# Kernel tuning notes

Measured on AMD Instinct MI355X. Metric: run time of the kernel, lower is better.

The kernel has to match this reference:

```python
import jax, jax.numpy as jnp
import numpy as np
from jax import lax

B, CIN, COUT, H, W, K = 8, 64, 64, 96, 96, 3
PAD = K // 2
EPS = 1e-5


def _conv(x, w, pad):
    return lax.conv_general_dilated(x, w, window_strides=(1, 1),
                                    padding=[(pad, pad), (pad, pad)],
                                    dimension_numbers=('NCHW', 'OIHW', 'NCHW'))


def setup_inputs() -> dict:
    key = jax.random.key(0)
    ks = jax.random.split(key, 7)
    x = jax.random.normal(ks[0], (B, CIN, H, W), dtype=jnp.float32)
    # offset conv (zero-init in the original; use small random weights so offsets are nontrivial)
    w_off = jax.random.normal(ks[1], (2 * K * K, CIN, K, K), dtype=jnp.float32) * 0.01
    b_off = jax.random.normal(ks[2], (2 * K * K,), dtype=jnp.float32) * 0.01
    w_def = jax.random.normal(ks[3], (COUT, CIN, K, K), dtype=jnp.float32) * (1.0 / np.sqrt(CIN * K * K))
    b_def = jax.random.normal(ks[4], (COUT,), dtype=jnp.float32) * 0.01
    gamma = jax.random.normal(ks[5], (COUT,), dtype=jnp.float32) * 0.1 + 1.0
    beta = jax.random.normal(ks[6], (COUT,), dtype=jnp.float32) * 0.1
    return {"x": x, "w_off": w_off, "b_off": b_off, "w_def": w_def,
            "b_def": b_def, "gamma": gamma, "beta": beta}


def _deform_block(x, w_off, b_off, w_def, b_def, gamma, beta):
    # 1) predict offsets: [B, 2*K*K, H, W]; channel 2k = dy, 2k+1 = dx for tap k=ky*K+kx
    offset = _conv(x, w_off, PAD) + b_off[None, :, None, None]
    dy = offset[:, 0::2]  # [B, K*K, H, W]
    dx = offset[:, 1::2]

    # 2) sampling positions p = p0 + p_k + dp (stride 1, zero-padding semantics)
    yy = jnp.arange(H, dtype=jnp.float32)[:, None]          # [H,1]
    xx = jnp.arange(W, dtype=jnp.float32)[None, :]          # [1,W]
    kk = jnp.arange(K * K)
    ky = (kk // K - PAD).astype(jnp.float32)[None, :, None, None]
    kx = (kk % K - PAD).astype(jnp.float32)[None, :, None, None]
    py = yy[None, None] + ky + dy                            # [B, K*K, H, W]
    px = xx[None, None] + kx + dx

    # 3) bilinear gather with zero outside-boundary
    y0 = jnp.floor(py); x0 = jnp.floor(px)
    ly = py - y0; lx = px - x0
    x_flat = x.reshape(B, CIN, H * W)
    sampled = jnp.zeros((B, CIN, K * K, H, W), dtype=x.dtype)
    for iy, wy in ((y0, 1.0 - ly), (y0 + 1.0, ly)):
        for ix, wx in ((x0, 1.0 - lx), (x0 + 1.0, lx)):
            valid = (iy >= 0) & (iy < H) & (ix >= 0) & (ix < W)
            yi = jnp.clip(iy, 0, H - 1).astype(jnp.int32)
            xi = jnp.clip(ix, 0, W - 1).astype(jnp.int32)
            idx = (yi * W + xi).reshape(B, -1)               # [B, K*K*H*W]
            vals = jnp.take_along_axis(x_flat, idx[:, None, :], axis=2)
            vals = vals.reshape(B, CIN, K * K, H, W)
            wgt = (wy * wx * valid.astype(x.dtype))[:, None]  # [B,1,K*K,H,W]
            sampled = sampled + vals * wgt

    # 4) deformable conv = contraction of sampled taps with kernel weights
    out = jnp.einsum('bckhw,ock->bohw', sampled, w_def.reshape(COUT, CIN, K * K))
    out = out + b_def[None, :, None, None]

    # 5) BatchNorm (training-mode batch statistics) + ReLU
    mean = jnp.mean(out, axis=(0, 2, 3))
    var = jnp.var(out, axis=(0, 2, 3))
    out = (out - mean[None, :, None, None]) * lax.rsqrt(var + EPS)[None, :, None, None]
    out = out * gamma[None, :, None, None] + beta[None, :, None, None]
    return jax.nn.relu(out)


def reference(x, w_off, b_off, w_def, b_def, gamma, beta):
    return _deform_block(x, w_off, b_off, w_def, b_def, gamma, beta)
```

## Files before the change

### kernel.cpp

```cpp
#include <hip/hip_runtime.h>

#define Hh 96
#define Ww 96
#define CIN 64
#define COUT 64
#define BATCH 8
#define HW 9216
#define NOFF 18

#define XS_ROW   13824
#define XS_SIZE  124416
#define WS_BASE  124416
#define OF_BASE  147744
#define SM_TOTAL 159264

typedef __attribute__((ext_vector_type(8))) short bf16x8;
typedef __attribute__((ext_vector_type(4))) float f32x4;

__device__ inline ushort f2bf(float f) {
  union { float f; uint u; } v; v.f = f;
  uint u = v.u;
  u += 0x7FFF + ((u >> 16) & 1);
  return (ushort)(u >> 16);
}
__device__ inline float bf2f(ushort s) {
  union { uint u; float f; } v; v.u = ((uint)s) << 16; return v.f;
}
__device__ inline float bflo(uint u) {
  union { uint u; float f; } v; v.u = u << 16; return v.f;
}
__device__ inline float bfhi(uint u) {
  union { uint u; float f; } v; v.u = u & 0xFFFF0000u; return v.f;
}
__device__ inline uint cvtpk(float lo, float hi) {
  uint r;
  asm("v_cvt_pk_bf16_f32 %0, %1, %2" : "=v"(r) : "v"(lo), "v"(hi));
  return r;
}
__device__ inline uint interp_pack(uint p00, uint p01, uint p10, uint p11,
                                   float w00, float w01, float w10, float w11) {
  float vlo = fmaf(w11, bflo(p11), fmaf(w10, bflo(p10),
              fmaf(w01, bflo(p01), w00 * bflo(p00))));
  float vhi = fmaf(w11, bfhi(p11), fmaf(w10, bfhi(p10),
              fmaf(w01, bfhi(p01), w00 * bfhi(p00))));
  return cvtpk(vlo, vhi);
}

__global__ __launch_bounds__(256) void k_xt(
    const float* __restrict__ x, const float* __restrict__ w_def,
    const float* __restrict__ w_off, ushort* __restrict__ xt,
    ushort* __restrict__ wtb, ushort* __restrict__ wob)
{
  __shared__ float tile[64][65];
  int tid = threadIdx.x;
  int blk = blockIdx.x;

  if (blk < 9) {
    for (int i = tid; i < 4096; i += 256) {
      int o = i >> 6, c = i & 63;
      wtb[blk * 4096 + i] = f2bf(w_def[(o * 64 + c) * 9 + blk]);
    }
  } else if (blk < 25 && blk >= 16) {
    int k = blk - 16;
    for (int i = tid; i < 2048; i += 256) {
      int n = i >> 6, c = i & 63;
      wob[k * 2048 + i] = (n < NOFF) ? f2bf(w_off[(n * 64 + c) * 9 + k]) : (ushort)0;
    }
  }

  int b = blk / 144;
  int pbase = (blk - b * 144) * 64;
  int wave = tid >> 6, lane = tid & 63;
  const float* xp = x + (size_t)b * CIN * HW + pbase;
  #pragma unroll
  for (int i = 0; i < 16; ++i) {
    int c = wave * 16 + i;
    tile[lane][c] = xp[(size_t)c * HW + lane];
  }
  __syncthreads();
  ushort* xo = xt + ((size_t)b * HW + pbase) * 64;
  #pragma unroll
  for (int i = 0; i < 16; ++i) {
    int p = wave * 16 + i;
    xo[(size_t)p * 64 + lane] = f2bf(tile[p][lane]);
  }
}

__global__ __launch_bounds__(768, 3) void k_main(
    const ushort* __restrict__ xt, const ushort* __restrict__ wtb,
    const ushort* __restrict__ wob, const float* __restrict__ b_off,
    const float* __restrict__ b_def, float* __restrict__ out,
    float* __restrict__ parts)
{
  extern __shared__ char sm[];
  int tid = threadIdx.x;
  int bid = blockIdx.x;
  int b = bid & 7;
  int rt = bid >> 3;
  int r0 = rt * 3;

  {
    const ushort* xsrc = xt + (size_t)b * HW * 64;
    for (int q = tid; q < 6912; q += 768) {
      int s = q / 768;
      int rem = q - s * 768;
      int cxp = rem >> 3, c16 = rem & 7;
      int srow = min(max(r0 - 3 + s, 0), 95);
      uint4 v = *(const uint4*)(xsrc + (size_t)(srow * 96 + cxp) * 64 + c16 * 8);
      *(uint4*)(sm + s * XS_ROW + cxp * 144 + c16 * 16) = v;
    }
  }
  for (int q = tid; q < 1296; q += 768) {
    int k = q / 144;
    int rem = q - k * 144;
    int n = rem >> 3, c16 = rem & 7;
    uint4 v = *(const uint4*)(wob + k * 2048 + n * 64 + c16 * 8);
    *(uint4*)(sm + WS_BASE + k * 2592 + n * 144 + c16 * 16) = v;
  }
  __syncthreads();

  int wave = tid >> 6, lane = tid & 63;
  int m = lane & 15, hi = lane >> 4;
  int kh = wave & 1;
  int gb = wave >> 1;
  int khB = kh * 64, hiB = hi * 16;

  int hA[3], wAc[3], pPix[3], gV[3];
  #pragma unroll
  for (int ti = 0; ti < 3; ++ti) {
    int g = gb + ti * 6;
    gV[ti] = g;
    int gr = g / 6, gc = g - gr * 6;
    hA[ti] = r0 + gr;
    wAc[ti] = gc * 16 + m;
    pPix[ti] = g * 16 + m;
  }

  f32x4 oacc[3][2];
  #pragma unroll
  for (int ti = 0; ti < 3; ++ti) {
    oacc[ti][0] = (f32x4){0.f, 0.f, 0.f, 0.f};
    oacc[ti][1] = (f32x4){0.f, 0.f, 0.f, 0.f};
  }
  for (int k = 0; k < 9; ++k) {
    int ky = k / 3 - 1, kx = (k - (k / 3) * 3) - 1;
    const char* wkb = sm + WS_BASE + k * 2592;
    bf16x8 wb0 = *(const bf16x8*)(wkb + m * 144 + hiB + khB);
    int r1 = min(16 + m, 17);
    bf16x8 wb1 = *(const bf16x8*)(wkb + r1 * 144 + hiB + khB);
    #pragma unroll
    for (int ti = 0; ti < 3; ++ti) {
      int yy = hA[ti] + ky, xx = wAc[ti] + kx;
      bool valid = (yy >= 0 && yy < Hh && xx >= 0 && xx < Ww);
      int cy = min(max(yy, 0), 95), cx = min(max(xx, 0), 95);
      int sy = cy - r0 + 3;
      bf16x8 a = *(const bf16x8*)(sm + sy * XS_ROW + cx * 144 + hiB + khB);
      if (!valid) a = (bf16x8)0;
      oacc[ti][0] = __builtin_amdgcn_mfma_f32_16x16x32_bf16(a, wb0, oacc[ti][0], 0, 0, 0);
      oacc[ti][1] = __builtin_amdgcn_mfma_f32_16x16x32_bf16(a, wb1, oacc[ti][1], 0, 0, 0);
    }
  }

  int j0 = m, j1 = 16 + m;
  if (kh == 1) {
    #pragma unroll
    for (int ti = 0; ti < 3; ++ti) {
      #pragma unroll
      for (int r = 0; r < 4; ++r) {
        int p = gV[ti] * 16 + hi * 4 + r;
        *(ushort*)(sm + OF_BASE + p * 40 + j0 * 2) = f2bf(oacc[ti][0][r]);
        if (m < 2)
          *(ushort*)(sm + OF_BASE + p * 40 + j1 * 2) = f2bf(oacc[ti][1][r]);
      }
    }
  }
  __syncthreads();
  if (kh == 0) {
    float bo0 = b_off[j0];
    float bo1 = (m < 2) ? b_off[j1] : 0.f;
    #pragma unroll
    for (int ti = 0; ti < 3; ++ti) {
      #pragma unroll
      for (int r = 0; r < 4; ++r) {
        int p = gV[ti] * 16 + hi * 4 + r;
        ushort* a0p = (ushort*)(sm + OF_BASE + p * 40 + j0 * 2);
        *a0p = f2bf(oacc[ti][0][r] + bf2f(*a0p) + bo0);
        if (m < 2) {
          ushort* a1p = (ushort*)(sm + OF_BASE + p * 40 + j1 * 2);
          *a1p = f2bf(oacc[ti][1][r] + bf2f(*a1p) + bo1);
        }
      }
    }
  }
  if (tid < 512) {
    int o = tid >> 3, c16 = tid & 7;
    uint4 v = *(const uint4*)(wtb + o * 64 + c16 * 8);
    *(uint4*)(sm + WS_BASE + o * 144 + c16 * 16) = v;
  }
  __syncthreads();

  f32x4 acc[3][4];
  #pragma unroll
  for (int ti = 0; ti < 3; ++ti)
    #pragma unroll
    for (int nt = 0; nt < 4; ++nt) acc[ti][nt] = (f32x4){0.f, 0.f, 0.f, 0.f};

  for (int k = 0; k < 9; ++k) {
    if (k < 8 && tid < 512) {
      int o = tid >> 3, c16 = tid & 7;
      uint4 v = *(const uint4*)(wtb + (k + 1) * 4096 + o * 64 + c16 * 8);
      *(uint4*)(sm + WS_BASE + ((k + 1) & 1) * 9216 + o * 144 + c16 * 16) = v;
    }
    int ky = k / 3 - 1, kx = (k - (k / 3) * 3) - 1;
    const char* wkb = sm + WS_BASE + (k & 1) * 9216;
    bf16x8 bf0 = *(const bf16x8*)(wkb + m * 144 + hiB + khB);
    bf16x8 bf1 = *(const bf16x8*)(wkb + (16 + m) * 144 + hiB + khB);
    bf16x8 bf2 = *(const bf16x8*)(wkb + (32 + m) * 144 + hiB + khB);
    bf16x8 bf3 = *(const bf16x8*)(wkb + (48 + m) * 144 + hiB + khB);

    #pragma unroll
    for (int ti = 0; ti < 3; ++ti) {
      uint dd = *(const uint*)(sm + OF_BASE + pPix[ti] * 40 + k * 4);
      float dy = bflo(dd), dx = bfhi(dd);
      float py = (float)(hA[ti] + ky) + dy;
      float px = (float)(wAc[ti] + kx) + dx;
      float y0f = floorf(py), x0f = floorf(px);
      float ly = py - y0f, lx = px - x0f;
      int y0 = (int)y0f, x0 = (int)x0f;
      int y1 = y0 + 1, x1 = x0 + 1;
      float fy0 = (y0 >= 0 && y0 < Hh) ? 1.f : 0.f;
      float fy1 = (y1 >= 0 && y1 < Hh) ? 1.f : 0.f;
      float fx0 = (x0 >= 0 && x0 < Ww) ? 1.f : 0.f;
      float fx1 = (x1 >= 0 && x1 < Ww) ? 1.f : 0.f;
      int cy0 = min(max(y0, 0), 95), cy1 = min(max(y1, 0), 95);
      int cx0 = min(max(x0, 0), 95), cx1 = min(max(x1, 0), 95);
      int sy0 = min(max(cy0 - r0 + 3, 0), 8);
      int sy1 = min(max(cy1 - r0 + 3, 0), 8);
      const char* row0 = sm + sy0 * XS_ROW;
      const char* row1 = sm + sy1 * XS_ROW;
      uint4 c00 = *(const uint4*)(row0 + cx0 * 144 + hiB + khB);
      uint4 c01 = *(const uint4*)(row0 + cx1 * 144 + hiB + khB);
      uint4 c10 = *(const uint4*)(row1 + cx0 * 144 + hiB + khB);
      uint4 c11 = *(const uint4*)(row1 + cx1 * 144 + hiB + khB);
      float w00 = (1.f - ly) * (1.f - lx) * (fy0 * fx0);
      float w01 = (1.f - ly) * lx * (fy0 * fx1);
      float w10 = ly * (1.f - lx) * (fy1 * fx0);
      float w11 = ly * lx * (fy1 * fx1);
      uint ua[4];
      ua[0] = interp_pack(c00.x, c01.x, c10.x, c11.x, w00, w01, w10, w11);
      ua[1] = interp_pack(c00.y, c01.y, c10.y, c11.y, w00, w01, w10, w11);
      ua[2] = interp_pack(c00.z, c01.z, c10.z, c11.z, w00, w01, w10, w11);
      ua[3] = interp_pack(c00.w, c01.w, c10.w, c11.w, w00, w01, w10, w11);
      bf16x8 av;
      __builtin_memcpy(&av, ua, 16);
      acc[ti][0] = __builtin_amdgcn_mfma_f32_16x16x32_bf16(av, bf0, acc[ti][0], 0, 0, 0);
      acc[ti][1] = __builtin_amdgcn_mfma_f32_16x16x32_bf16(av, bf1, acc[ti][1], 0, 0, 0);
      acc[ti][2] = __builtin_amdgcn_mfma_f32_16x16x32_bf16(av, bf2, acc[ti][2], 0, 0, 0);
      acc[ti][3] = __builtin_amdgcn_mfma_f32_16x16x32_bf16(av, bf3, acc[ti][3], 0, 0, 0);
    }
    __syncthreads();
  }

  float* T = (float*)sm;
  if (kh == 1) {
    #pragma unroll
    for (int ti = 0; ti < 3; ++ti)
      #pragma unroll
      for (int nt = 0; nt < 4; ++nt) {
        int o = nt * 16 + m;
        #pragma unroll
        for (int r = 0; r < 4; ++r) {
          int p = gV[ti] * 16 + hi * 4 + r;
          T[o * 289 + p] = acc[ti][nt][r];
        }
      }
  }
  __syncthreads();
  if (kh == 0) {
    float bd[4];
    bd[0] = b_def[m]; bd[1] = b_def[16 + m];
    bd[2] = b_def[32 + m]; bd[3] = b_def[48 + m];
    #pragma unroll
    for (int ti = 0; ti < 3; ++ti)
      #pragma unroll
      for (int nt = 0; nt < 4; ++nt) {
        int o = nt * 16 + m;
        #pragma unroll
        for (int r = 0; r < 4; ++r) {
          int p = gV[ti] * 16 + hi * 4 + r;
          T[o * 289 + p] += acc[ti][nt][r] + bd[nt];
        }
      }
  }
  __syncthreads();
  if (tid < 512) {
    int o = tid >> 3, seg = tid & 7;
    const float* Tr = T + o * 289 + seg * 36;
    float* og = out + ((size_t)(b * 64 + o)) * HW + rt * 288 + seg * 36;
    float s = 0.f, ss = 0.f;
    #pragma unroll
    for (int j4 = 0; j4 < 9; ++j4) {
      float4 v;
      v.x = Tr[j4 * 4 + 0]; v.y = Tr[j4 * 4 + 1];
      v.z = Tr[j4 * 4 + 2]; v.w = Tr[j4 * 4 + 3];
      s += v.x + v.y + v.z + v.w;
      ss += v.x * v.x + v.y * v.y + v.z * v.z + v.w * v.w;
      *(float4*)(og + j4 * 4) = v;
    }
    s += __shfl_down(s, 4); s += __shfl_down(s, 2); s += __shfl_down(s, 1);
    ss += __shfl_down(ss, 4); ss += __shfl_down(ss, 2); ss += __shfl_down(ss, 1);
    if ((tid & 7) == 0) {
      parts[o * 256 + bid] = s;
      parts[16384 + o * 256 + bid] = ss;
    }
  }
}

__global__ __launch_bounds__(256) void k_stats(
    const float* __restrict__ parts, const float* __restrict__ gamma,
    const float* __restrict__ beta, float* __restrict__ stats)
{
  int c = blockIdx.x;
  int tid = threadIdx.x;
  float s = 0.f, ss = 0.f;
  for (int i = tid; i < 256; i += 256) {
    s += parts[c * 256 + i];
    ss += parts[16384 + c * 256 + i];
  }
  #pragma unroll
  for (int off = 32; off >= 1; off >>= 1) {
    s += __shfl_down(s, off);
    ss += __shfl_down(ss, off);
  }
  __shared__ float rs[4], rss[4];
  int wave = tid >> 6, lane = tid & 63;
  if (lane == 0) { rs[wave] = s; rss[wave] = ss; }
  __syncthreads();
  if (tid == 0) {
    float S1 = rs[0] + rs[1] + rs[2] + rs[3];
    float S2 = rss[0] + rss[1] + rss[2] + rss[3];
    const float inv = 1.f / 73728.f;
    float mean = S1 * inv;
    float var = S2 * inv - mean * mean;
    float scale = gamma[c] * rsqrtf(var + 1e-5f);
    stats[c] = scale;
    stats[64 + c] = beta[c] - mean * scale;
  }
}

__global__ __launch_bounds__(256) void k_norm(
    float* __restrict__ out, const float* __restrict__ stats)
{
  int g = blockIdx.x * 256 + threadIdx.x;
  int o = (g / 2304) & 63;
  float sc = stats[o], sh = stats[64 + o];
  float4 v = ((const float4*)out)[g];
  v.x = fmaxf(fmaf(v.x, sc, sh), 0.f);
  v.y = fmaxf(fmaf(v.y, sc, sh), 0.f);
  v.z = fmaxf(fmaf(v.z, sc, sh), 0.f);
  v.w = fmaxf(fmaf(v.w, sc, sh), 0.f);
  ((float4*)out)[g] = v;
}

extern "C" void kernel_launch(void* const* d_in, const int* in_sizes, int n_in,
                              void* d_out, int out_size, void* d_ws, size_t ws_size,
                              hipStream_t stream) {
  const float* x     = (const float*)d_in[0];
  const float* w_off = (const float*)d_in[1];
  const float* b_off = (const float*)d_in[2];
  const float* w_def = (const float*)d_in[3];
  const float* b_def = (const float*)d_in[4];
  const float* gamma = (const float*)d_in[5];
  const float* beta  = (const float*)d_in[6];
  float* out = (float*)d_out;

  float* base  = (float*)d_ws;
  ushort* wtb  = (ushort*)base;
  ushort* wob  = (ushort*)(base + 18432);
  ushort* xt   = (ushort*)(base + 18432 + 9216);
  float* parts = base + 18432 + 9216 + 2359296;
  float* stats = parts + 32768;

  (void)hipFuncSetAttribute((const void*)k_main,
      hipFuncAttributeMaxDynamicSharedMemorySize, SM_TOTAL);

  k_xt<<<1152, 256, 0, stream>>>(x, w_def, w_off, xt, wtb, wob);
  k_main<<<256, 768, SM_TOTAL, stream>>>(xt, wtb, wob, b_off, b_def, out, parts);
  k_stats<<<64, 256, 0, stream>>>(parts, gamma, beta, stats);
  k_norm<<<4608, 256, 0, stream>>>(out, stats);
}
```

Measured before the change: 59.95 us.

## Fuse NCHW-to-bf16 transpose into main kernel and read weights from global

Drops the separate transpose kernel that wrote a channels-last bf16 copy of x. The main kernel now loads fp32 x straight from NCHW global memory, converts it to bf16 and stores it into its shared-memory tile. Weight fragments for both the offset and the deform convolutions are read directly from global memory instead of being staged through shared memory, which frees LDS and removes the per-tap barrier. The bilinear interpolation now uses packed fp32 FMA instructions. The trade-offs are strided per-channel global loads during staging and weight reads that depend on cache hits.

```diff
diff --git a/kernel.cpp b/kernel.cpp
--- a/kernel.cpp
+++ b/kernel.cpp
@@ -10,12 +10,12 @@
 
 #define XS_ROW   13824
 #define XS_SIZE  124416
-#define WS_BASE  124416
-#define OF_BASE  147744
-#define SM_TOTAL 159264
+#define OF_BASE  124416
+#define SM_TOTAL 135936
 
 typedef __attribute__((ext_vector_type(8))) short bf16x8;
 typedef __attribute__((ext_vector_type(4))) float f32x4;
+typedef __attribute__((ext_vector_type(2))) float f32x2;
 
 __device__ inline ushort f2bf(float f) {
   union { float f; uint u; } v; v.f = f;
@@ -26,68 +26,45 @@
 __device__ inline float bf2f(ushort s) {
   union { uint u; float f; } v; v.u = ((uint)s) << 16; return v.f;
 }
-__device__ inline float bflo(uint u) {
-  union { uint u; float f; } v; v.u = u << 16; return v.f;
-}
-__device__ inline float bfhi(uint u) {
-  union { uint u; float f; } v; v.u = u & 0xFFFF0000u; return v.f;
-}
 __device__ inline uint cvtpk(float lo, float hi) {
   uint r;
   asm("v_cvt_pk_bf16_f32 %0, %1, %2" : "=v"(r) : "v"(lo), "v"(hi));
   return r;
 }
-__device__ inline uint interp_pack(uint p00, uint p01, uint p10, uint p11,
-                                   float w00, float w01, float w10, float w11) {
-  float vlo = fmaf(w11, bflo(p11), fmaf(w10, bflo(p10),
-              fmaf(w01, bflo(p01), w00 * bflo(p00))));
-  float vhi = fmaf(w11, bfhi(p11), fmaf(w10, bfhi(p10),
-              fmaf(w01, bfhi(p01), w00 * bfhi(p00))));
-  return cvtpk(vlo, vhi);
-}
-
-__global__ __launch_bounds__(256) void k_xt(
-    const float* __restrict__ x, const float* __restrict__ w_def,
-    const float* __restrict__ w_off, ushort* __restrict__ xt,
+__device__ inline f32x2 unpack2(uint u) {
+  union { uint u[2]; f32x2 f; } r;
+  r.u[0] = u << 16; r.u[1] = u & 0xFFFF0000u;
+  return r.f;
+}
+__device__ inline f32x2 pkfma(f32x2 a, f32x2 b, f32x2 c) {
+  f32x2 d;
+  asm("v_pk_fma_f32 %0, %1, %2, %3" : "=v"(d) : "v"(a), "v"(b), "v"(c));
+  return d;
+}
+__device__ inline f32x2 pkmul(f32x2 a, f32x2 b) {
+  f32x2 d;
+  asm("v_pk_mul_f32 %0, %1, %2" : "=v"(d) : "v"(a), "v"(b));
+  return d;
+}
+
+__global__ __launch_bounds__(256) void k_wpack(
+    const float* __restrict__ w_def, const float* __restrict__ w_off,
     ushort* __restrict__ wtb, ushort* __restrict__ wob)
 {
-  __shared__ float tile[64][65];
-  int tid = threadIdx.x;
-  int blk = blockIdx.x;
-
-  if (blk < 9) {
-    for (int i = tid; i < 4096; i += 256) {
-      int o = i >> 6, c = i & 63;
-      wtb[blk * 4096 + i] = f2bf(w_def[(o * 64 + c) * 9 + blk]);
-    }
-  } else if (blk < 25 && blk >= 16) {
-    int k = blk - 16;
-    for (int i = tid; i < 2048; i += 256) {
-      int n = i >> 6, c = i & 63;
-      wob[k * 2048 + i] = (n < NOFF) ? f2bf(w_off[(n * 64 + c) * 9 + k]) : (ushort)0;
-    }
-  }
-
-  int b = blk / 144;
-  int pbase = (blk - b * 144) * 64;
-  int wave = tid >> 6, lane = tid & 63;
-  const float* xp = x + (size_t)b * CIN * HW + pbase;
-  #pragma unroll
-  for (int i = 0; i < 16; ++i) {
-    int c = wave * 16 + i;
-    tile[lane][c] = xp[(size_t)c * HW + lane];
-  }
-  __syncthreads();
-  ushort* xo = xt + ((size_t)b * HW + pbase) * 64;
-  #pragma unroll
-  for (int i = 0; i < 16; ++i) {
-    int p = wave * 16 + i;
-    xo[(size_t)p * 64 + lane] = f2bf(tile[p][lane]);
+  int g = blockIdx.x * 256 + threadIdx.x;
+  if (g < 36864) {
+    int k = g >> 12, o = (g >> 6) & 63, c = g & 63;
+    wtb[g] = f2bf(w_def[(o * 64 + c) * 9 + k]);
+  }
+  int g2 = g - 36864;
+  if (g2 >= 0 && g2 < 18432) {
+    int k = g2 >> 11, n = (g2 >> 6) & 31, c = g2 & 63;
+    wob[g2] = (n < NOFF) ? f2bf(w_off[(n * 64 + c) * 9 + k]) : (ushort)0;
   }
 }
 
 __global__ __launch_bounds__(768, 3) void k_main(
-    const ushort* __restrict__ xt, const ushort* __restrict__ wtb,
+    const float* __restrict__ x, const ushort* __restrict__ wtb,
     const ushort* __restrict__ wob, const float* __restrict__ b_off,
     const float* __restrict__ b_def, float* __restrict__ out,
     float* __restrict__ parts)
@@ -100,22 +77,20 @@
   int r0 = rt * 3;
 
   {
-    const ushort* xsrc = xt + (size_t)b * HW * 64;
-    for (int q = tid; q < 6912; q += 768) {
-      int s = q / 768;
-      int rem = q - s * 768;
-      int cxp = rem >> 3, c16 = rem & 7;
+    const float* xb_g = x + (size_t)b * CIN * HW;
+    int px = tid >> 3, cg = tid & 7;
+    #pragma unroll
+    for (int s = 0; s < 9; ++s) {
       int srow = min(max(r0 - 3 + s, 0), 95);
-      uint4 v = *(const uint4*)(xsrc + (size_t)(srow * 96 + cxp) * 64 + c16 * 8);
-      *(uint4*)(sm + s * XS_ROW + cxp * 144 + c16 * 16) = v;
-    }
-  }
-  for (int q = tid; q < 1296; q += 768) {
-    int k = q / 144;
-    int rem = q - k * 144;
-    int n = rem >> 3, c16 = rem & 7;
-    uint4 v = *(const uint4*)(wob + k * 2048 + n * 64 + c16 * 8);
-    *(uint4*)(sm + WS_BASE + k * 2592 + n * 144 + c16 * 16) = v;
+      const float* src = xb_g + (size_t)(cg * 8) * HW + srow * 96 + px;
+      float v[8];
+      #pragma unroll
+      for (int j = 0; j < 8; ++j) v[j] = src[(size_t)j * HW];
+      uint u[4];
+      u[0] = cvtpk(v[0], v[1]); u[1] = cvtpk(v[2], v[3]);
+      u[2] = cvtpk(v[4], v[5]); u[3] = cvtpk(v[6], v[7]);
+      *(uint4*)(sm + s * XS_ROW + px * 144 + cg * 16) = *(uint4*)u;
+    }
   }
   __syncthreads();
 
@@ -124,6 +99,7 @@
   int kh = wave & 1;
   int gb = wave >> 1;
   int khB = kh * 64, hiB = hi * 16;
+  int chE = kh * 32 + hi * 8;
 
   int hA[3], wAc[3], pPix[3], gV[3];
   #pragma unroll
@@ -144,10 +120,9 @@
   }
   for (int k = 0; k < 9; ++k) {
     int ky = k / 3 - 1, kx = (k - (k / 3) * 3) - 1;
-    const char* wkb = sm + WS_BASE + k * 2592;
-    bf16x8 wb0 = *(const bf16x8*)(wkb + m * 144 + hiB + khB);
-    int r1 = min(16 + m, 17);
-    bf16x8 wb1 = *(const bf16x8*)(wkb + r1 * 144 + hiB + khB);
+    const ushort* wk = wob + k * 2048 + chE;
+    bf16x8 wb0 = *(const bf16x8*)(wk + m * 64);
+    bf16x8 wb1 = *(const bf16x8*)(wk + (16 + m) * 64);
     #pragma unroll
     for (int ti = 0; ti < 3; ++ti) {
       int yy = hA[ti] + ky, xx = wAc[ti] + kx;
@@ -192,11 +167,6 @@
       }
     }
   }
-  if (tid < 512) {
-    int o = tid >> 3, c16 = tid & 7;
-    uint4 v = *(const uint4*)(wtb + o * 64 + c16 * 8);
-    *(uint4*)(sm + WS_BASE + o * 144 + c16 * 16) = v;
-  }
   __syncthreads();
 
   f32x4 acc[3][4];
@@ -206,24 +176,19 @@
     for (int nt = 0; nt < 4; ++nt) acc[ti][nt] = (f32x4){0.f, 0.f, 0.f, 0.f};
 
   for (int k = 0; k < 9; ++k) {
-    if (k < 8 && tid < 512) {
-      int o = tid >> 3, c16 = tid & 7;
-      uint4 v = *(const uint4*)(wtb + (k + 1) * 4096 + o * 64 + c16 * 8);
-      *(uint4*)(sm + WS_BASE + ((k + 1) & 1) * 9216 + o * 144 + c16 * 16) = v;
-    }
     int ky = k / 3 - 1, kx = (k - (k / 3) * 3) - 1;
-    const char* wkb = sm + WS_BASE + (k & 1) * 9216;
-    bf16x8 bf0 = *(const bf16x8*)(wkb + m * 144 + hiB + khB);
-    bf16x8 bf1 = *(const bf16x8*)(wkb + (16 + m) * 144 + hiB + khB);
-    bf16x8 bf2 = *(const bf16x8*)(wkb + (32 + m) * 144 + hiB + khB);
-    bf16x8 bf3 = *(const bf16x8*)(wkb + (48 + m) * 144 + hiB + khB);
+    const ushort* wk = wtb + k * 4096 + chE;
+    bf16x8 bf0 = *(const bf16x8*)(wk + m * 64);
+    bf16x8 bf1 = *(const bf16x8*)(wk + (16 + m) * 64);
+    bf16x8 bf2 = *(const bf16x8*)(wk + (32 + m) * 64);
+    bf16x8 bf3 = *(const bf16x8*)(wk + (48 + m) * 64);
 
     #pragma unroll
     for (int ti = 0; ti < 3; ++ti) {
       uint dd = *(const uint*)(sm + OF_BASE + pPix[ti] * 40 + k * 4);
-      float dy = bflo(dd), dx = bfhi(dd);
-      float py = (float)(hA[ti] + ky) + dy;
-      float px = (float)(wAc[ti] + kx) + dx;
+      f32x2 dpair = unpack2(dd);
+      float py = (float)(hA[ti] + ky) + dpair.x;
+      float px = (float)(wAc[ti] + kx) + dpair.y;
       float y0f = floorf(py), x0f = floorf(px);
       float ly = py - y0f, lx = px - x0f;
       int y0 = (int)y0f, x0 = (int)x0f;
@@ -242,15 +207,25 @@
       uint4 c01 = *(const uint4*)(row0 + cx1 * 144 + hiB + khB);
       uint4 c10 = *(const uint4*)(row1 + cx0 * 144 + hiB + khB);
       uint4 c11 = *(const uint4*)(row1 + cx1 * 144 + hiB + khB);
-      float w00 = (1.f - ly) * (1.f - lx) * (fy0 * fx0);
-      float w01 = (1.f - ly) * lx * (fy0 * fx1);
-      float w10 = ly * (1.f - lx) * (fy1 * fx0);
-      float w11 = ly * lx * (fy1 * fx1);
+      float s00 = (1.f - ly) * (1.f - lx) * (fy0 * fx0);
+      float s01 = (1.f - ly) * lx * (fy0 * fx1);
+      float s10 = ly * (1.f - lx) * (fy1 * fx0);
+      float s11 = ly * lx * (fy1 * fx1);
+      f32x2 w00 = (f32x2){s00, s00}, w01 = (f32x2){s01, s01};
+      f32x2 w10 = (f32x2){s10, s10}, w11 = (f32x2){s11, s11};
       uint ua[4];
-      ua[0] = interp_pack(c00.x, c01.x, c10.x, c11.x, w00, w01, w10, w11);
-      ua[1] = interp_pack(c00.y, c01.y, c10.y, c11.y, w00, w01, w10, w11);
-      ua[2] = interp_pack(c00.z, c01.z, c10.z, c11.z, w00, w01, w10, w11);
-      ua[3] = interp_pack(c00.w, c01.w, c10.w, c11.w, w00, w01, w10, w11);
+      {
+        const uint* p00 = (const uint*)&c00; const uint* p01 = (const uint*)&c01;
+        const uint* p10 = (const uint*)&c10; const uint* p11 = (const uint*)&c11;
+        #pragma unroll
+        for (int q = 0; q < 4; ++q) {
+          f32x2 sv = pkmul(w00, unpack2(p00[q]));
+          sv = pkfma(w01, unpack2(p01[q]), sv);
+          sv = pkfma(w10, unpack2(p10[q]), sv);
+          sv = pkfma(w11, unpack2(p11[q]), sv);
+          ua[q] = cvtpk(sv.x, sv.y);
+        }
+      }
       bf16x8 av;
       __builtin_memcpy(&av, ua, 16);
       acc[ti][0] = __builtin_amdgcn_mfma_f32_16x16x32_bf16(av, bf0, acc[ti][0], 0, 0, 0);
@@ -258,8 +233,8 @@
       acc[ti][2] = __builtin_amdgcn_mfma_f32_16x16x32_bf16(av, bf2, acc[ti][2], 0, 0, 0);
       acc[ti][3] = __builtin_amdgcn_mfma_f32_16x16x32_bf16(av, bf3, acc[ti][3], 0, 0, 0);
     }
-    __syncthreads();
-  }
+  }
+  __syncthreads();
 
   float* T = (float*)sm;
   if (kh == 1) {
@@ -323,9 +298,9 @@
   int c = blockIdx.x;
   int tid = threadIdx.x;
   float s = 0.f, ss = 0.f;
-  for (int i = tid; i < 256; i += 256) {
-    s += parts[c * 256 + i];
-    ss += parts[16384 + c * 256 + i];
+  if (tid < 256) {
+    s = parts[c * 256 + tid];
+    ss = parts[16384 + c * 256 + tid];
   }
   #pragma unroll
   for (int off = 32; off >= 1; off >>= 1) {
@@ -377,15 +352,14 @@
   float* base  = (float*)d_ws;
   ushort* wtb  = (ushort*)base;
   ushort* wob  = (ushort*)(base + 18432);
-  ushort* xt   = (ushort*)(base + 18432 + 9216);
-  float* parts = base + 18432 + 9216 + 2359296;
+  float* parts = base + 18432 + 9216;
   float* stats = parts + 32768;
 
   (void)hipFuncSetAttribute((const void*)k_main,
       hipFuncAttributeMaxDynamicSharedMemorySize, SM_TOTAL);
 
-  k_xt<<<1152, 256, 0, stream>>>(x, w_def, w_off, xt, wtb, wob);
-  k_main<<<256, 768, SM_TOTAL, stream>>>(xt, wtb, wob, b_off, b_def, out, parts);
+  k_wpack<<<216, 256, 0, stream>>>(w_def, w_off, wtb, wob);
+  k_main<<<256, 768, SM_TOTAL, stream>>>(x, wtb, wob, b_off, b_def, out, parts);
   k_stats<<<64, 256, 0, stream>>>(parts, gamma, beta, stats);
   k_norm<<<4608, 256, 0, stream>>>(out, stats);
 }
```

Measured after the change: 70.66 us. +17.9%, slower.

## Fuse NCHW-to-NHWC bf16 transpose of x into main kernel's LDS staging load

Applied to the files above, without the earlier changes.

Removes the separate k_xt pass that transposed x into a channels-last bf16 buffer in global memory. k_main now reads fp32 x directly in NCHW layout, converts pairs to bf16 and writes the channel-interleaved tile into shared memory itself. The weight packing moves to a small dedicated kernel. This saves one full write and read of the transposed activation plus a launch, at the cost of strided per-channel fp32 global loads inside k_main and redundant reads of halo rows across tiles.

```diff
diff --git a/kernel.cpp b/kernel.cpp
--- a/kernel.cpp
+++ b/kernel.cpp
@@ -46,48 +46,24 @@
   return cvtpk(vlo, vhi);
 }
 
-__global__ __launch_bounds__(256) void k_xt(
-    const float* __restrict__ x, const float* __restrict__ w_def,
-    const float* __restrict__ w_off, ushort* __restrict__ xt,
+__global__ __launch_bounds__(256) void k_wpack(
+    const float* __restrict__ w_def, const float* __restrict__ w_off,
     ushort* __restrict__ wtb, ushort* __restrict__ wob)
 {
-  __shared__ float tile[64][65];
-  int tid = threadIdx.x;
-  int blk = blockIdx.x;
-
-  if (blk < 9) {
-    for (int i = tid; i < 4096; i += 256) {
-      int o = i >> 6, c = i & 63;
-      wtb[blk * 4096 + i] = f2bf(w_def[(o * 64 + c) * 9 + blk]);
-    }
-  } else if (blk < 25 && blk >= 16) {
-    int k = blk - 16;
-    for (int i = tid; i < 2048; i += 256) {
-      int n = i >> 6, c = i & 63;
-      wob[k * 2048 + i] = (n < NOFF) ? f2bf(w_off[(n * 64 + c) * 9 + k]) : (ushort)0;
-    }
-  }
-
-  int b = blk / 144;
-  int pbase = (blk - b * 144) * 64;
-  int wave = tid >> 6, lane = tid & 63;
-  const float* xp = x + (size_t)b * CIN * HW + pbase;
-  #pragma unroll
-  for (int i = 0; i < 16; ++i) {
-    int c = wave * 16 + i;
-    tile[lane][c] = xp[(size_t)c * HW + lane];
-  }
-  __syncthreads();
-  ushort* xo = xt + ((size_t)b * HW + pbase) * 64;
-  #pragma unroll
-  for (int i = 0; i < 16; ++i) {
-    int p = wave * 16 + i;
-    xo[(size_t)p * 64 + lane] = f2bf(tile[p][lane]);
+  int g = blockIdx.x * 256 + threadIdx.x;
+  if (g < 36864) {
+    int k = g >> 12, o = (g >> 6) & 63, c = g & 63;
+    wtb[g] = f2bf(w_def[(o * 64 + c) * 9 + k]);
+  }
+  int g2 = g - 36864;
+  if (g2 >= 0 && g2 < 18432) {
+    int k = g2 >> 11, n = (g2 >> 6) & 31, c = g2 & 63;
+    wob[g2] = (n < NOFF) ? f2bf(w_off[(n * 64 + c) * 9 + k]) : (ushort)0;
   }
 }
 
 __global__ __launch_bounds__(768, 3) void k_main(
-    const ushort* __restrict__ xt, const ushort* __restrict__ wtb,
+    const float* __restrict__ x, const ushort* __restrict__ wtb,
     const ushort* __restrict__ wob, const float* __restrict__ b_off,
     const float* __restrict__ b_def, float* __restrict__ out,
     float* __restrict__ parts)
@@ -100,14 +76,19 @@
   int r0 = rt * 3;
 
   {
-    const ushort* xsrc = xt + (size_t)b * HW * 64;
-    for (int q = tid; q < 6912; q += 768) {
-      int s = q / 768;
-      int rem = q - s * 768;
-      int cxp = rem >> 3, c16 = rem & 7;
+    const float* xb_g = x + (size_t)b * CIN * HW;
+    int px = tid >> 3, cg = tid & 7;
+    #pragma unroll
+    for (int s = 0; s < 9; ++s) {
       int srow = min(max(r0 - 3 + s, 0), 95);
-      uint4 v = *(const uint4*)(xsrc + (size_t)(srow * 96 + cxp) * 64 + c16 * 8);
-      *(uint4*)(sm + s * XS_ROW + cxp * 144 + c16 * 16) = v;
+      const float* src = xb_g + (size_t)(cg * 8) * HW + srow * 96 + px;
+      float v[8];
+      #pragma unroll
+      for (int j = 0; j < 8; ++j) v[j] = src[(size_t)j * HW];
+      uint u[4];
+      u[0] = cvtpk(v[0], v[1]); u[1] = cvtpk(v[2], v[3]);
+      u[2] = cvtpk(v[4], v[5]); u[3] = cvtpk(v[6], v[7]);
+      *(uint4*)(sm + s * XS_ROW + px * 144 + cg * 16) = *(uint4*)u;
     }
   }
   for (int q = tid; q < 1296; q += 768) {
@@ -377,15 +358,14 @@
   float* base  = (float*)d_ws;
   ushort* wtb  = (ushort*)base;
   ushort* wob  = (ushort*)(base + 18432);
-  ushort* xt   = (ushort*)(base + 18432 + 9216);
-  float* parts = base + 18432 + 9216 + 2359296;
+  float* parts = base + 18432 + 9216;
   float* stats = parts + 32768;
 
   (void)hipFuncSetAttribute((const void*)k_main,
       hipFuncAttributeMaxDynamicSharedMemorySize, SM_TOTAL);
 
-  k_xt<<<1152, 256, 0, stream>>>(x, w_def, w_off, xt, wtb, wob);
-  k_main<<<256, 768, SM_TOTAL, stream>>>(xt, wtb, wob, b_off, b_def, out, parts);
+  k_wpack<<<216, 256, 0, stream>>>(w_def, w_off, wtb, wob);
+  k_main<<<256, 768, SM_TOTAL, stream>>>(x, wtb, wob, b_off, b_def, out, parts);
   k_stats<<<64, 256, 0, stream>>>(parts, gamma, beta, stats);
   k_norm<<<4608, 256, 0, stream>>>(out, stats);
 }
```

Measured after the change: 67.90 us. 1.13x slower.
